# Kernel optimization log

Hardware: AMD Instinct MI355X
Metric: run time of the kernel (lower is better)

## Reference

```python
import jax, jax.numpy as jnp
import numpy as np

B, S, D_MODEL, H, D_K, D_V = 2, 2048, 1024, 16, 64, 64


def setup_inputs() -> dict:
    key = jax.random.key(0)
    ks = jax.random.split(key, 12)
    s = 0.02
    inp = {
        "Q": jax.random.normal(ks[0], (B, S, D_MODEL), jnp.float32),
        "K": jax.random.normal(ks[1], (B, S, D_MODEL), jnp.float32),
        "V": jax.random.normal(ks[2], (B, S, D_MODEL), jnp.float32),
        # causal 0/1 mask, broadcastable to [B, H, S, S]
        "mask": jnp.tril(jnp.ones((S, S), jnp.int32))[None, None, :, :],
        "Wq": jax.random.normal(ks[3], (D_MODEL, H * D_K), jnp.float32) * s,
        "bq": jnp.zeros((H * D_K,), jnp.float32),
        "Wk": jax.random.normal(ks[4], (D_MODEL, H * D_K), jnp.float32) * s,
        "bk": jnp.zeros((H * D_K,), jnp.float32),
        "Wv": jax.random.normal(ks[5], (D_MODEL, H * D_V), jnp.float32) * s,
        "bv": jnp.zeros((H * D_V,), jnp.float32),
        "Wo": jax.random.normal(ks[6], (H * D_V, D_MODEL), jnp.float32) * s,
        "bo": jnp.zeros((D_MODEL,), jnp.float32),
    }
    return inp


def reference(Q, K, V, mask, Wq, bq, Wk, bk, Wv, bv, Wo, bo):
    b = Q.shape[0]
    # project and split heads: [B, S, H*dk] -> [B, H, S, dk]
    q = (Q @ Wq + bq).reshape(b, -1, H, D_K).transpose(0, 2, 1, 3)
    k = (K @ Wk + bk).reshape(b, -1, H, D_K).transpose(0, 2, 1, 3)
    v = (V @ Wv + bv).reshape(b, -1, H, D_V).transpose(0, 2, 1, 3)
    scale = 1.0 / np.sqrt(D_K).astype(np.float32)
    scores = jnp.einsum("bhqd,bhkd->bhqk", q, k) * scale
    scores = jnp.where(mask == 0, jnp.float32(-1e9), scores)
    attn = jax.nn.softmax(scores, axis=-1)
    context = jnp.einsum("bhqk,bhkd->bhqd", attn, v)
    context = context.transpose(0, 2, 1, 3).reshape(b, -1, H * D_V)
    output = context @ Wo + bo  # dropout is identity in eval
    return output, attn
```

## Files before the change

### kernel.cpp

```cpp
#include <hip/hip_runtime.h>
#include <math.h>

#define S_LEN 2048
#define DMODEL 1024
#define NHEAD 16
#define HD 64
#define NBATCH 2

using short8  = __attribute__((ext_vector_type(8))) short;
using ushort8 = __attribute__((ext_vector_type(8))) unsigned short;
using floatx4 = __attribute__((ext_vector_type(4))) float;

__device__ __forceinline__ unsigned short f2b(float f) {
    unsigned int u = __float_as_uint(f);
    unsigned int r = (u + 0x7FFFu + ((u >> 16) & 1u)) >> 16;
    return (unsigned short)r;
}

__device__ __forceinline__ void gll16(const void* g, void* l) {
    __builtin_amdgcn_global_load_lds(
        (const __attribute__((address_space(1))) unsigned int*)g,
        (__attribute__((address_space(3))) unsigned int*)l, 16, 0, 0);
}

__global__ __launch_bounds__(256)
void convert_bf16(const float* __restrict__ S0, const float* __restrict__ S1,
                  const float* __restrict__ S2,
                  unsigned short* __restrict__ D0, unsigned short* __restrict__ D1,
                  unsigned short* __restrict__ D2, int n4)
{
    const float* src = (blockIdx.z == 0) ? S0 : (blockIdx.z == 1) ? S1 : S2;
    unsigned short* dst = (blockIdx.z == 0) ? D0 : (blockIdx.z == 1) ? D1 : D2;
    int i = blockIdx.x * 256 + threadIdx.x;
    if (i < n4) {
        float4 v = ((const float4*)src)[i];
        ushort4 o;
        o.x = f2b(v.x); o.y = f2b(v.y); o.z = f2b(v.z); o.w = f2b(v.w);
        ((ushort4*)dst)[i] = o;
    }
}

__global__ __launch_bounds__(256)
void transpose_w(const float* __restrict__ W0, const float* __restrict__ W1,
                 const float* __restrict__ W2, const float* __restrict__ W3,
                 unsigned short* __restrict__ T0, unsigned short* __restrict__ T1,
                 unsigned short* __restrict__ T2, unsigned short* __restrict__ T3)
{
    __shared__ float t[64][65];
    const float* W; unsigned short* T;
    switch (blockIdx.z) {
        case 0: W = W0; T = T0; break;
        case 1: W = W1; T = T1; break;
        case 2: W = W2; T = T2; break;
        default: W = W3; T = T3; break;
    }
    const int tid = threadIdx.x;
    const int c0 = blockIdx.x * 64;
    const int r0 = blockIdx.y * 64;
    #pragma unroll
    for (int i = 0; i < 4; ++i) {
        int c = tid + i * 256;
        int r = c >> 4, off = (c & 15) * 4;
        float4 v = *(const float4*)(W + (size_t)(r0 + r) * DMODEL + c0 + off);
        t[r][off + 0] = v.x; t[r][off + 1] = v.y;
        t[r][off + 2] = v.z; t[r][off + 3] = v.w;
    }
    __syncthreads();
    #pragma unroll
    for (int i = 0; i < 4; ++i) {
        int c = tid + i * 256;
        int n = c >> 4, off = (c & 15) * 4;
        ushort4 o;
        o.x = f2b(t[off + 0][n]); o.y = f2b(t[off + 1][n]);
        o.z = f2b(t[off + 2][n]); o.w = f2b(t[off + 3][n]);
        *(ushort4*)(T + (size_t)(c0 + n) * DMODEL + r0 + off) = o;
    }
}

__global__ __launch_bounds__(256)
void gemm_qkv(const unsigned short* __restrict__ X0, const unsigned short* __restrict__ X1,
              const unsigned short* __restrict__ X2,
              const unsigned short* __restrict__ W0, const unsigned short* __restrict__ W1,
              const unsigned short* __restrict__ W2,
              const float* __restrict__ b0, const float* __restrict__ b1,
              const float* __restrict__ b2,
              unsigned short* __restrict__ o0, unsigned short* __restrict__ o1,
              unsigned short* __restrict__ o2)
{
    __shared__ unsigned short Xs[128 * 64];
    __shared__ unsigned short Ws[128 * 64];

    const unsigned short* X  = (blockIdx.z == 0) ? X0 : (blockIdx.z == 1) ? X1 : X2;
    const unsigned short* Wt = (blockIdx.z == 0) ? W0 : (blockIdx.z == 1) ? W1 : W2;
    const float* bias        = (blockIdx.z == 0) ? b0 : (blockIdx.z == 1) ? b1 : b2;
    unsigned short* outp     = (blockIdx.z == 0) ? o0 : (blockIdx.z == 1) ? o1 : o2;

    const int tid = threadIdx.x;
    const int lane = tid & 63, w = tid >> 6;
    const int l15 = lane & 15, l4 = lane >> 4;
    const int wr = w >> 1, wc = w & 1;
    const int row0 = blockIdx.y * 128;
    const int col0 = blockIdx.x * 128;

    const int srow = lane >> 3;
    const int sblk = (lane & 7) ^ srow;

    floatx4 acc[4][4] = {};

    for (int k0 = 0; k0 < DMODEL; k0 += 64) {
        __syncthreads();
        #pragma unroll
        for (int i = 0; i < 4; ++i)
            gll16(X + (size_t)(row0 + w * 32 + i * 8 + srow) * DMODEL + k0 + sblk * 8,
                  &Xs[(w * 32 + i * 8) * 64]);
        #pragma unroll
        for (int i = 0; i < 4; ++i)
            gll16(Wt + (size_t)(col0 + w * 32 + i * 8 + srow) * DMODEL + k0 + sblk * 8,
                  &Ws[(w * 32 + i * 8) * 64]);
        asm volatile("s_waitcnt vmcnt(0)" ::: "memory");
        __syncthreads();

        #pragma unroll
        for (int ks = 0; ks < 2; ++ks) {
            short8 a[4], b[4];
            #pragma unroll
            for (int m = 0; m < 4; ++m) {
                const int r = wr * 64 + m * 16 + l15;
                a[m] = *(const short8*)&Xs[r * 64 + (((ks * 4 + l4) ^ (r & 7)) << 3)];
            }
            #pragma unroll
            for (int n = 0; n < 4; ++n) {
                const int r = wc * 64 + n * 16 + l15;
                b[n] = *(const short8*)&Ws[r * 64 + (((ks * 4 + l4) ^ (r & 7)) << 3)];
            }
            #pragma unroll
            for (int m = 0; m < 4; ++m)
                #pragma unroll
                for (int n = 0; n < 4; ++n)
                    acc[m][n] = __builtin_amdgcn_mfma_f32_16x16x32_bf16(
                        a[m], b[n], acc[m][n], 0, 0, 0);
        }
    }

    float bl[4];
    #pragma unroll
    for (int n = 0; n < 4; ++n)
        bl[n] = bias[col0 + wc * 64 + n * 16 + l15];

    #pragma unroll
    for (int m = 0; m < 4; ++m)
        #pragma unroll
        for (int n = 0; n < 4; ++n) {
            const int gc = col0 + wc * 64 + n * 16 + l15;
            const int h = gc >> 6, d = gc & 63;
            #pragma unroll
            for (int reg = 0; reg < 4; ++reg) {
                const int gr = row0 + wr * 64 + m * 16 + l4 * 4 + reg;
                const int bb = gr >> 11, s = gr & 2047;
                outp[(((size_t)bb * NHEAD + h) * S_LEN + s) * HD + d] =
                    f2b(acc[m][n][reg] + bl[n]);
            }
        }
}

__global__ __launch_bounds__(256)
void gemm_out(const unsigned short* __restrict__ X, const unsigned short* __restrict__ Wt,
              const float* __restrict__ bias, float* __restrict__ out)
{
    __shared__ unsigned short Xs[128 * 64];
    __shared__ unsigned short Ws[128 * 64];

    const int tid = threadIdx.x;
    const int lane = tid & 63, w = tid >> 6;
    const int l15 = lane & 15, l4 = lane >> 4;
    const int wr = w >> 1, wc = w & 1;
    const int row0 = blockIdx.y * 128;
    const int col0 = blockIdx.x * 128;

    const int srow = lane >> 3;
    const int sblk = (lane & 7) ^ srow;

    floatx4 acc[4][4] = {};

    for (int k0 = 0; k0 < DMODEL; k0 += 64) {
        __syncthreads();
        #pragma unroll
        for (int i = 0; i < 4; ++i)
            gll16(X + (size_t)(row0 + w * 32 + i * 8 + srow) * DMODEL + k0 + sblk * 8,
                  &Xs[(w * 32 + i * 8) * 64]);
        #pragma unroll
        for (int i = 0; i < 4; ++i)
            gll16(Wt + (size_t)(col0 + w * 32 + i * 8 + srow) * DMODEL + k0 + sblk * 8,
                  &Ws[(w * 32 + i * 8) * 64]);
        asm volatile("s_waitcnt vmcnt(0)" ::: "memory");
        __syncthreads();

        #pragma unroll
        for (int ks = 0; ks < 2; ++ks) {
            short8 a[4], b[4];
            #pragma unroll
            for (int m = 0; m < 4; ++m) {
                const int r = wr * 64 + m * 16 + l15;
                a[m] = *(const short8*)&Xs[r * 64 + (((ks * 4 + l4) ^ (r & 7)) << 3)];
            }
            #pragma unroll
            for (int n = 0; n < 4; ++n) {
                const int r = wc * 64 + n * 16 + l15;
                b[n] = *(const short8*)&Ws[r * 64 + (((ks * 4 + l4) ^ (r & 7)) << 3)];
            }
            #pragma unroll
            for (int m = 0; m < 4; ++m)
                #pragma unroll
                for (int n = 0; n < 4; ++n)
                    acc[m][n] = __builtin_amdgcn_mfma_f32_16x16x32_bf16(
                        a[m], b[n], acc[m][n], 0, 0, 0);
        }
    }

    float bl[4];
    #pragma unroll
    for (int n = 0; n < 4; ++n)
        bl[n] = bias[col0 + wc * 64 + n * 16 + l15];

    #pragma unroll
    for (int m = 0; m < 4; ++m)
        #pragma unroll
        for (int n = 0; n < 4; ++n) {
            const int gc = col0 + wc * 64 + n * 16 + l15;
            #pragma unroll
            for (int reg = 0; reg < 4; ++reg) {
                const int gr = row0 + wr * 64 + m * 16 + l4 * 4 + reg;
                out[(size_t)gr * DMODEL + gc] = acc[m][n][reg] + bl[n];
            }
        }
}

__device__ __forceinline__ int vt_off(int d, int jblk) {
    return d * 64 + ((jblk ^ ((d ^ (d >> 3)) & 7)) << 3);
}

__global__ __launch_bounds__(256)
void attn_mfma(const unsigned short* __restrict__ qg, const unsigned short* __restrict__ kg,
               const unsigned short* __restrict__ vg, float* __restrict__ attn,
               unsigned short* __restrict__ ctx)
{
    __shared__ unsigned short Ks[64 * 64];
    __shared__ unsigned short Vt[64 * 64];
    __shared__ unsigned short Ps[64 * 88];

    const int tid = threadIdx.x;
    const int lane = tid & 63, w = tid >> 6;
    const int l15 = lane & 15, l4 = lane >> 4;

    const int i0 = blockIdx.x;
    const int local = i0 >> 3;
    const int bh = (i0 & 7) * 4 + (local & 3);
    const int qx = local >> 2;
    const int qb = (bh & 1) ? (31 - qx) : qx;
    const int row0 = qb * 64;

    const int srow = lane >> 3;
    const int sblk = (lane & 7) ^ srow;

    const float C2 = 0.18033688011112042f;

    const unsigned short* qh = qg + (size_t)bh * S_LEN * HD;
    const unsigned short* kh = kg + (size_t)bh * S_LEN * HD;
    const unsigned short* vh = vg + (size_t)bh * S_LEN * HD;
    float* attnh = attn + (size_t)bh * S_LEN * S_LEN;

    short8 qa[2];
    #pragma unroll
    for (int ks = 0; ks < 2; ++ks)
        qa[ks] = *(const short8*)(qh + (size_t)(row0 + w * 16 + l15) * HD + ks * 32 + l4 * 8);

    const int nt = qb + 1;

    float lsum[4] = {};
    for (int jt = 0; jt < nt; ++jt) {
        __syncthreads();
        #pragma unroll
        for (int i = 0; i < 2; ++i)
            gll16(kh + (size_t)(jt * 64 + w * 16 + i * 8 + srow) * HD + sblk * 8,
                  &Ks[(w * 16 + i * 8) * 64]);
        asm volatile("s_waitcnt vmcnt(0)" ::: "memory");
        __syncthreads();

        floatx4 sf[4] = {};
        #pragma unroll
        for (int ks = 0; ks < 2; ++ks) {
            short8 kb[4];
            #pragma unroll
            for (int c = 0; c < 4; ++c) {
                const int r = c * 16 + l15;
                kb[c] = *(const short8*)&Ks[r * 64 + (((ks * 4 + l4) ^ (r & 7)) << 3)];
            }
            #pragma unroll
            for (int c = 0; c < 4; ++c)
                sf[c] = __builtin_amdgcn_mfma_f32_16x16x32_bf16(qa[ks], kb[c], sf[c], 0, 0, 0);
        }

        const int rbase = row0 + w * 16;
        if (jt * 64 + 63 <= rbase) {
            #pragma unroll
            for (int c = 0; c < 4; ++c)
                #pragma unroll
                for (int reg = 0; reg < 4; ++reg)
                    lsum[reg] += exp2f(sf[c][reg] * C2);
        } else {
            #pragma unroll
            for (int c = 0; c < 4; ++c) {
                const int jcol = jt * 64 + c * 16 + l15;
                #pragma unroll
                for (int reg = 0; reg < 4; ++reg) {
                    const int grow = rbase + l4 * 4 + reg;
                    lsum[reg] += (jcol <= grow) ? exp2f(sf[c][reg] * C2) : 0.f;
                }
            }
        }
    }

    float nl2[4];
    #pragma unroll
    for (int reg = 0; reg < 4; ++reg) {
        float s = lsum[reg];
        #pragma unroll
        for (int off = 1; off < 16; off <<= 1)
            s += __shfl_xor(s, off);
        nl2[reg] = -__log2f(s);
    }

    floatx4 o[4] = {};
    for (int jt = 0; jt < nt; ++jt) {
        __syncthreads();
        const int jj0 = tid >> 3, d0v = (tid & 7) * 8;
        ushort8 vva = *(const ushort8*)(vh + (size_t)(jt * 64 + jj0) * HD + d0v);
        ushort8 vvb = *(const ushort8*)(vh + (size_t)(jt * 64 + jj0 + 32) * HD + d0v);
        #pragma unroll
        for (int i = 0; i < 2; ++i)
            gll16(kh + (size_t)(jt * 64 + w * 16 + i * 8 + srow) * HD + sblk * 8,
                  &Ks[(w * 16 + i * 8) * 64]);
        #pragma unroll
        for (int e = 0; e < 8; ++e) {
            Vt[vt_off(d0v + e, jj0 >> 3) + (jj0 & 7)] = vva[e];
            Vt[vt_off(d0v + e, (jj0 + 32) >> 3) + ((jj0 + 32) & 7)] = vvb[e];
        }
        asm volatile("s_waitcnt vmcnt(0)" ::: "memory");
        __syncthreads();

        floatx4 sf[4] = {};
        #pragma unroll
        for (int ks = 0; ks < 2; ++ks) {
            short8 kb[4];
            #pragma unroll
            for (int c = 0; c < 4; ++c) {
                const int r = c * 16 + l15;
                kb[c] = *(const short8*)&Ks[r * 64 + (((ks * 4 + l4) ^ (r & 7)) << 3)];
            }
            #pragma unroll
            for (int c = 0; c < 4; ++c)
                sf[c] = __builtin_amdgcn_mfma_f32_16x16x32_bf16(qa[ks], kb[c], sf[c], 0, 0, 0);
        }

        const int rbase = row0 + w * 16;
        const bool full = (jt * 64 + 63 <= rbase);
        #pragma unroll
        for (int c = 0; c < 4; ++c) {
            const int jcol = jt * 64 + c * 16 + l15;
            #pragma unroll
            for (int reg = 0; reg < 4; ++reg) {
                const int rl = w * 16 + l4 * 4 + reg;
                float p = exp2f(fmaf(sf[c][reg], C2, nl2[reg]));
                if (!full && jcol > rbase + l4 * 4 + reg) p = 0.f;
                attnh[(size_t)(row0 + rl) * S_LEN + jcol] = p;
                Ps[rl * 88 + c * 16 + l15] = f2b(p);
            }
        }
        __syncthreads();

        #pragma unroll
        for (int ks = 0; ks < 2; ++ks) {
            const short8 pa = *(const short8*)&Ps[(w * 16 + l15) * 88 + ks * 32 + l4 * 8];
            #pragma unroll
            for (int c = 0; c < 4; ++c) {
                const short8 vb = *(const short8*)&Vt[vt_off(c * 16 + l15, ks * 4 + l4)];
                o[c] = __builtin_amdgcn_mfma_f32_16x16x32_bf16(pa, vb, o[c], 0, 0, 0);
            }
        }
    }

    const int b = bh >> 4, h = bh & 15;
    #pragma unroll
    for (int c = 0; c < 4; ++c)
        #pragma unroll
        for (int reg = 0; reg < 4; ++reg) {
            const int gr = row0 + w * 16 + l4 * 4 + reg;
            const int d = c * 16 + l15;
            ctx[((size_t)b * S_LEN + gr) * DMODEL + h * HD + d] = f2b(o[c][reg]);
        }

    const float4 z4 = {0.f, 0.f, 0.f, 0.f};
    for (int jt = nt; jt < S_LEN / 64; ++jt) {
        #pragma unroll
        for (int i = 0; i < 4; ++i) {
            const int idx = tid + i * 256;
            const int r = idx >> 4, off = (idx & 15) * 4;
            *(float4*)(attnh + (size_t)(row0 + r) * S_LEN + jt * 64 + off) = z4;
        }
    }
}

extern "C" void kernel_launch(void* const* d_in, const int* in_sizes, int n_in,
                              void* d_out, int out_size, void* d_ws, size_t ws_size,
                              hipStream_t stream)
{
    const float* Q  = (const float*)d_in[0];
    const float* K  = (const float*)d_in[1];
    const float* V  = (const float*)d_in[2];
    const float* Wq = (const float*)d_in[4];
    const float* bq = (const float*)d_in[5];
    const float* Wk = (const float*)d_in[6];
    const float* bk = (const float*)d_in[7];
    const float* Wv = (const float*)d_in[8];
    const float* bv = (const float*)d_in[9];
    const float* Wo = (const float*)d_in[10];
    const float* bo = (const float*)d_in[11];

    float* out  = (float*)d_out;
    float* attn = out + (size_t)NBATCH * S_LEN * DMODEL;

    const size_t per = (size_t)NBATCH * S_LEN * DMODEL;
    const size_t wsz = (size_t)DMODEL * DMODEL;
    unsigned short* Xq  = (unsigned short*)d_ws;
    unsigned short* Xk  = Xq + per;
    unsigned short* Xv  = Xk + per;
    unsigned short* Wtq = Xv + per;
    unsigned short* Wtk = Wtq + wsz;
    unsigned short* Wtv = Wtk + wsz;
    unsigned short* Wto = Wtv + wsz;
    unsigned short* qhw = Wto + wsz;
    unsigned short* khw = qhw + per;
    unsigned short* vhw = khw + per;
    unsigned short* ctx = vhw + per;

    const int n4 = (int)(per / 4);
    convert_bf16<<<dim3((n4 + 255) / 256, 1, 3), 256, 0, stream>>>(
        Q, K, V, Xq, Xk, Xv, n4);
    transpose_w<<<dim3(16, 16, 4), 256, 0, stream>>>(Wq, Wk, Wv, Wo, Wtq, Wtk, Wtv, Wto);

    gemm_qkv<<<dim3(DMODEL / 128, (NBATCH * S_LEN) / 128, 3), 256, 0, stream>>>(
        Xq, Xk, Xv, Wtq, Wtk, Wtv, bq, bk, bv, qhw, khw, vhw);

    attn_mfma<<<1024, 256, 0, stream>>>(qhw, khw, vhw, attn, ctx);

    gemm_out<<<dim3(DMODEL / 128, (NBATCH * S_LEN) / 128), 256, 0, stream>>>(
        ctx, Wto, bo, out);
}
```

Before: 278.5 us.

## Double-buffer K/V tile loads in attention and narrow output GEMM tiles

The attention kernel now double-buffers K tiles in shared memory in both passes. The next tile is issued before the current one is computed, and the wait uses partial vmcnt counts instead of draining all loads. In the second pass the next V tile is also prefetched into registers, with a lambda alternating two register sets. Separately, the output GEMM moves to 128x64 tiles, doubling the block count for better CU occupancy at the cost of reloading the X operand more often. Together this adds shared-memory use and relies on in-order completion of the vmcnt counter.

```diff
diff --git a/kernel.cpp b/kernel.cpp
--- a/kernel.cpp
+++ b/kernel.cpp
@@ -168,19 +168,19 @@
               const float* __restrict__ bias, float* __restrict__ out)
 {
     __shared__ unsigned short Xs[128 * 64];
-    __shared__ unsigned short Ws[128 * 64];
+    __shared__ unsigned short Ws[64 * 64];
 
     const int tid = threadIdx.x;
     const int lane = tid & 63, w = tid >> 6;
     const int l15 = lane & 15, l4 = lane >> 4;
     const int wr = w >> 1, wc = w & 1;
     const int row0 = blockIdx.y * 128;
-    const int col0 = blockIdx.x * 128;
+    const int col0 = blockIdx.x * 64;
 
     const int srow = lane >> 3;
     const int sblk = (lane & 7) ^ srow;
 
-    floatx4 acc[4][4] = {};
+    floatx4 acc[4][2] = {};
 
     for (int k0 = 0; k0 < DMODEL; k0 += 64) {
         __syncthreads();
@@ -189,44 +189,44 @@
             gll16(X + (size_t)(row0 + w * 32 + i * 8 + srow) * DMODEL + k0 + sblk * 8,
                   &Xs[(w * 32 + i * 8) * 64]);
         #pragma unroll
-        for (int i = 0; i < 4; ++i)
-            gll16(Wt + (size_t)(col0 + w * 32 + i * 8 + srow) * DMODEL + k0 + sblk * 8,
-                  &Ws[(w * 32 + i * 8) * 64]);
+        for (int i = 0; i < 2; ++i)
+            gll16(Wt + (size_t)(col0 + w * 16 + i * 8 + srow) * DMODEL + k0 + sblk * 8,
+                  &Ws[(w * 16 + i * 8) * 64]);
         asm volatile("s_waitcnt vmcnt(0)" ::: "memory");
         __syncthreads();
 
         #pragma unroll
         for (int ks = 0; ks < 2; ++ks) {
-            short8 a[4], b[4];
+            short8 a[4], b[2];
             #pragma unroll
             for (int m = 0; m < 4; ++m) {
                 const int r = wr * 64 + m * 16 + l15;
                 a[m] = *(const short8*)&Xs[r * 64 + (((ks * 4 + l4) ^ (r & 7)) << 3)];
             }
             #pragma unroll
-            for (int n = 0; n < 4; ++n) {
-                const int r = wc * 64 + n * 16 + l15;
+            for (int n = 0; n < 2; ++n) {
+                const int r = wc * 32 + n * 16 + l15;
                 b[n] = *(const short8*)&Ws[r * 64 + (((ks * 4 + l4) ^ (r & 7)) << 3)];
             }
             #pragma unroll
             for (int m = 0; m < 4; ++m)
                 #pragma unroll
-                for (int n = 0; n < 4; ++n)
+                for (int n = 0; n < 2; ++n)
                     acc[m][n] = __builtin_amdgcn_mfma_f32_16x16x32_bf16(
                         a[m], b[n], acc[m][n], 0, 0, 0);
         }
     }
 
-    float bl[4];
-    #pragma unroll
-    for (int n = 0; n < 4; ++n)
-        bl[n] = bias[col0 + wc * 64 + n * 16 + l15];
+    float bl[2];
+    #pragma unroll
+    for (int n = 0; n < 2; ++n)
+        bl[n] = bias[col0 + wc * 32 + n * 16 + l15];
 
     #pragma unroll
     for (int m = 0; m < 4; ++m)
         #pragma unroll
-        for (int n = 0; n < 4; ++n) {
-            const int gc = col0 + wc * 64 + n * 16 + l15;
+        for (int n = 0; n < 2; ++n) {
+            const int gc = col0 + wc * 32 + n * 16 + l15;
             #pragma unroll
             for (int reg = 0; reg < 4; ++reg) {
                 const int gr = row0 + wr * 64 + m * 16 + l4 * 4 + reg;
@@ -244,7 +244,7 @@
                const unsigned short* __restrict__ vg, float* __restrict__ attn,
                unsigned short* __restrict__ ctx)
 {
-    __shared__ unsigned short Ks[64 * 64];
+    __shared__ unsigned short Ks[2 * 64 * 64];
     __shared__ unsigned short Vt[64 * 64];
     __shared__ unsigned short Ps[64 * 88];
 
@@ -275,15 +275,26 @@
         qa[ks] = *(const short8*)(qh + (size_t)(row0 + w * 16 + l15) * HD + ks * 32 + l4 * 8);
 
     const int nt = qb + 1;
+    const int jj0 = tid >> 3, d0v = (tid & 7) * 8;
+
+    #pragma unroll
+    for (int i = 0; i < 2; ++i)
+        gll16(kh + (size_t)(w * 16 + i * 8 + srow) * HD + sblk * 8,
+              &Ks[(w * 16 + i * 8) * 64]);
 
     float lsum[4] = {};
     for (int jt = 0; jt < nt; ++jt) {
-        __syncthreads();
-        #pragma unroll
-        for (int i = 0; i < 2; ++i)
-            gll16(kh + (size_t)(jt * 64 + w * 16 + i * 8 + srow) * HD + sblk * 8,
-                  &Ks[(w * 16 + i * 8) * 64]);
-        asm volatile("s_waitcnt vmcnt(0)" ::: "memory");
+        const int cur = jt & 1;
+        __syncthreads();
+        if (jt + 1 < nt) {
+            #pragma unroll
+            for (int i = 0; i < 2; ++i)
+                gll16(kh + (size_t)((jt + 1) * 64 + w * 16 + i * 8 + srow) * HD + sblk * 8,
+                      &Ks[(cur ^ 1) * 4096 + (w * 16 + i * 8) * 64]);
+            asm volatile("s_waitcnt vmcnt(2)" ::: "memory");
+        } else {
+            asm volatile("s_waitcnt vmcnt(0)" ::: "memory");
+        }
         __syncthreads();
 
         floatx4 sf[4] = {};
@@ -293,7 +304,8 @@
             #pragma unroll
             for (int c = 0; c < 4; ++c) {
                 const int r = c * 16 + l15;
-                kb[c] = *(const short8*)&Ks[r * 64 + (((ks * 4 + l4) ^ (r & 7)) << 3)];
+                kb[c] = *(const short8*)&Ks[cur * 4096 + r * 64
+                                            + (((ks * 4 + l4) ^ (r & 7)) << 3)];
             }
             #pragma unroll
             for (int c = 0; c < 4; ++c)
@@ -331,22 +343,37 @@
     }
 
     floatx4 o[4] = {};
-    for (int jt = 0; jt < nt; ++jt) {
-        __syncthreads();
-        const int jj0 = tid >> 3, d0v = (tid & 7) * 8;
-        ushort8 vva = *(const ushort8*)(vh + (size_t)(jt * 64 + jj0) * HD + d0v);
-        ushort8 vvb = *(const ushort8*)(vh + (size_t)(jt * 64 + jj0 + 32) * HD + d0v);
-        #pragma unroll
-        for (int i = 0; i < 2; ++i)
-            gll16(kh + (size_t)(jt * 64 + w * 16 + i * 8 + srow) * HD + sblk * 8,
-                  &Ks[(w * 16 + i * 8) * 64]);
+
+    __syncthreads();
+    #pragma unroll
+    for (int i = 0; i < 2; ++i)
+        gll16(kh + (size_t)(w * 16 + i * 8 + srow) * HD + sblk * 8,
+              &Ks[(w * 16 + i * 8) * 64]);
+    ushort8 vA0 = *(const ushort8*)(vh + (size_t)jj0 * HD + d0v);
+    ushort8 vA1 = *(const ushort8*)(vh + (size_t)(jj0 + 32) * HD + d0v);
+    ushort8 vB0, vB1;
+
+    auto p2_iter = [&](int jt, int buf, ushort8& vc0, ushort8& vc1,
+                       ushort8& vn0, ushort8& vn1) {
+        __syncthreads();
+        if (jt + 1 < nt) {
+            #pragma unroll
+            for (int i = 0; i < 2; ++i)
+                gll16(kh + (size_t)((jt + 1) * 64 + w * 16 + i * 8 + srow) * HD + sblk * 8,
+                      &Ks[(buf ^ 1) * 4096 + (w * 16 + i * 8) * 64]);
+            vn0 = *(const ushort8*)(vh + (size_t)((jt + 1) * 64 + jj0) * HD + d0v);
+            vn1 = *(const ushort8*)(vh + (size_t)((jt + 1) * 64 + jj0 + 32) * HD + d0v);
+            asm volatile("s_waitcnt vmcnt(4)" ::: "memory");
+        } else {
+            asm volatile("s_waitcnt vmcnt(0)" ::: "memory");
+        }
+        __syncthreads();
+
         #pragma unroll
         for (int e = 0; e < 8; ++e) {
-            Vt[vt_off(d0v + e, jj0 >> 3) + (jj0 & 7)] = vva[e];
-            Vt[vt_off(d0v + e, (jj0 + 32) >> 3) + ((jj0 + 32) & 7)] = vvb[e];
-        }
-        asm volatile("s_waitcnt vmcnt(0)" ::: "memory");
-        __syncthreads();
+            Vt[vt_off(d0v + e, jj0 >> 3) + (jj0 & 7)] = vc0[e];
+            Vt[vt_off(d0v + e, (jj0 + 32) >> 3) + ((jj0 + 32) & 7)] = vc1[e];
+        }
 
         floatx4 sf[4] = {};
         #pragma unroll
@@ -355,7 +382,8 @@
             #pragma unroll
             for (int c = 0; c < 4; ++c) {
                 const int r = c * 16 + l15;
-                kb[c] = *(const short8*)&Ks[r * 64 + (((ks * 4 + l4) ^ (r & 7)) << 3)];
+                kb[c] = *(const short8*)&Ks[buf * 4096 + r * 64
+                                            + (((ks * 4 + l4) ^ (r & 7)) << 3)];
             }
             #pragma unroll
             for (int c = 0; c < 4; ++c)
@@ -387,6 +415,12 @@
                 o[c] = __builtin_amdgcn_mfma_f32_16x16x32_bf16(pa, vb, o[c], 0, 0, 0);
             }
         }
+    };
+
+    for (int jt2 = 0; jt2 < nt; jt2 += 2) {
+        p2_iter(jt2, 0, vA0, vA1, vB0, vB1);
+        if (jt2 + 1 < nt)
+            p2_iter(jt2 + 1, 1, vB0, vB1, vA0, vA1);
     }
 
     const int b = bh >> 4, h = bh & 15;
@@ -453,6 +487,6 @@
 
     attn_mfma<<<1024, 256, 0, stream>>>(qhw, khw, vhw, attn, ctx);
 
-    gemm_out<<<dim3(DMODEL / 128, (NBATCH * S_LEN) / 128), 256, 0, stream>>>(
+    gemm_out<<<dim3(DMODEL / 64, (NBATCH * S_LEN) / 128), 256, 0, stream>>>(
         ctx, Wto, bo, out);
 }
```

After: 266.5 us. 1.04x faster.
